# Performance work log

Measured on AMD Instinct MI355X. Metric: run time of the kernel, lower is better.

## Reference

```python
import jax, jax.numpy as jnp
import numpy as np

INPUT_DIM = 2048
EMBED_DIM = 128


def setup_inputs() -> dict:
    key = jax.random.key(0)
    kx, kw, kb, kv = jax.random.split(key, 4)
    x = jax.random.normal(kx, (16384, INPUT_DIM), dtype=jnp.float32)
    # nn.Linear(input_dim, 1): weight [1, D] (init std=0.01), bias [1]
    W = jax.random.normal(kw, (1, INPUT_DIM), dtype=jnp.float32) * 0.01
    b = jax.random.normal(kb, (1,), dtype=jnp.float32) * 0.01
    # nn.Embedding(input_dim, embedding_dim): V [D, K] (init std=0.01)
    V = jax.random.normal(kv, (INPUT_DIM, EMBED_DIM), dtype=jnp.float32) * 0.01
    return {"x": x, "W": W, "b": b, "V": V}


def reference(x, W, b, V):
    # linear part: x @ W^T + b -> [B, 1]
    linear_part = x @ W.T + b
    # FM 2nd-order interaction via the standard identity:
    # 0.5 * sum_k ( (sum_d x_d V_dk)^2 - sum_d x_d^2 V_dk^2 )
    # equals the original sum_square - square_sum over weighted embeddings.
    xv = x @ V                       # [B, K]
    x2v2 = (x * x) @ (V * V)         # [B, K]
    interaction = 0.5 * jnp.sum(xv * xv - x2v2, axis=1, keepdims=True)
    return linear_part + interaction
```

## Files before the change

### kernel.cpp

```cpp
#include <hip/hip_runtime.h>
#include <hip/hip_bf16.h>

#define INPUT_DIM 2048
#define EMBED_DIM 128
#define NROWS 16384

typedef __bf16 bf16x8 __attribute__((ext_vector_type(8)));
typedef float f32x4 __attribute__((ext_vector_type(4)));

__device__ inline float dot4(f32x4 a, f32x4 b) {
    return a.x * b.x + a.y * b.y + a.z * b.z + a.w * b.w;
}

__global__ __launch_bounds__(256) void fm_prep(const float* __restrict__ V,
                                               __bf16* __restrict__ Vt,
                                               float* __restrict__ s) {
    const int bid = blockIdx.x;
    const int tid = threadIdx.x;
    if (bid < 128) {
        const int g = bid * 256 + tid;
        const int n = g & 127;
        const int kc = g >> 7;
        bf16x8 o;
#pragma unroll
        for (int e = 0; e < 8; ++e)
            o[e] = (__bf16)V[(kc * 8 + e) * EMBED_DIM + n];
        *(bf16x8*)(Vt + (size_t)n * INPUT_DIM + kc * 8) = o;
    } else {
        const int k = (bid - 128) * 256 + tid;
        const f32x4* row = (const f32x4*)(V + (size_t)k * EMBED_DIM);
        float acc = 0.f;
#pragma unroll
        for (int j = 0; j < EMBED_DIM / 4; ++j) {
            f32x4 v = row[j];
            acc += dot4(v, v);
        }
        s[k] = acc;
    }
}

__global__ __launch_bounds__(256, 4) void fm_main(const float* __restrict__ x,
                                                  const float* __restrict__ W,
                                                  const float* __restrict__ bptr,
                                                  const __bf16* __restrict__ Vt,
                                                  const float* __restrict__ s,
                                                  float* __restrict__ out) {
    __shared__ __align__(16) float acc_lds[4][16][132];
    __shared__ float lin_lds[4][16];
    __shared__ float sq_lds[4][16];

    const int tid = threadIdx.x;
    const int w = tid >> 6;
    const int l = tid & 63;
    const int lr = l & 15;
    const int lg = l >> 4;

    const int row0 = blockIdx.x * 16;
    const int k0 = w * 512;

    const float* xp = x + (size_t)(row0 + lr) * INPUT_DIM + k0 + lg * 8;
    const float* wp = W + k0 + lg * 8;
    const float* sp = s + k0 + lg * 8;
    const __bf16* vtp = Vt + (size_t)lr * INPUT_DIM + k0 + lg * 8;

    f32x4 acc[8];
#pragma unroll
    for (int c = 0; c < 8; ++c) acc[c] = (f32x4){0.f, 0.f, 0.f, 0.f};
    float lin = 0.f, sq = 0.f;

    for (int step = 0; step < 16; ++step) {
        f32x4 a0 = *(const f32x4*)xp;
        f32x4 a1 = *(const f32x4*)(xp + 4);
        f32x4 w0 = *(const f32x4*)wp;
        f32x4 w1 = *(const f32x4*)(wp + 4);
        f32x4 s0 = *(const f32x4*)sp;
        f32x4 s1 = *(const f32x4*)(sp + 4);
        xp += 32; wp += 32; sp += 32;

        lin += dot4(a0, w0) + dot4(a1, w1);
        sq += dot4(a0 * a0, s0) + dot4(a1 * a1, s1);

        bf16x8 af;
        af[0] = (__bf16)a0.x; af[1] = (__bf16)a0.y;
        af[2] = (__bf16)a0.z; af[3] = (__bf16)a0.w;
        af[4] = (__bf16)a1.x; af[5] = (__bf16)a1.y;
        af[6] = (__bf16)a1.z; af[7] = (__bf16)a1.w;

#pragma unroll
        for (int c = 0; c < 8; ++c) {
            bf16x8 bf = *(const bf16x8*)(vtp + (size_t)c * 16 * INPUT_DIM);
            acc[c] = __builtin_amdgcn_mfma_f32_16x16x32_bf16(af, bf, acc[c], 0, 0, 0);
        }
        vtp += 32;
    }

#pragma unroll
    for (int c = 0; c < 8; ++c)
#pragma unroll
        for (int r = 0; r < 4; ++r)
            acc_lds[w][lg * 4 + r][c * 16 + lr] = acc[c][r];

    lin += __shfl_xor(lin, 16); lin += __shfl_xor(lin, 32);
    sq  += __shfl_xor(sq, 16);  sq  += __shfl_xor(sq, 32);
    if (l < 16) { lin_lds[w][l] = lin; sq_lds[w][l] = sq; }
    __syncthreads();

    {
        const int row = tid >> 4;
        const int nc = (tid & 15) * 8;
        f32x4 v0 = (f32x4){0.f, 0.f, 0.f, 0.f};
        f32x4 v1 = (f32x4){0.f, 0.f, 0.f, 0.f};
#pragma unroll
        for (int ww = 0; ww < 4; ++ww) {
            v0 += *(const f32x4*)&acc_lds[ww][row][nc];
            v1 += *(const f32x4*)&acc_lds[ww][row][nc + 4];
        }
        float ss = dot4(v0, v0) + dot4(v1, v1);
        ss += __shfl_xor(ss, 1);
        ss += __shfl_xor(ss, 2);
        ss += __shfl_xor(ss, 4);
        ss += __shfl_xor(ss, 8);
        if ((tid & 15) == 0) {
            float linf = lin_lds[0][row] + lin_lds[1][row] + lin_lds[2][row] + lin_lds[3][row];
            float sqf  = sq_lds[0][row] + sq_lds[1][row] + sq_lds[2][row] + sq_lds[3][row];
            out[row0 + row] = linf + bptr[0] + 0.5f * (ss - sqf);
        }
    }
}

extern "C" void kernel_launch(void* const* d_in, const int* in_sizes, int n_in,
                              void* d_out, int out_size, void* d_ws, size_t ws_size,
                              hipStream_t stream) {
    const float* x = (const float*)d_in[0];
    const float* W = (const float*)d_in[1];
    const float* b = (const float*)d_in[2];
    const float* V = (const float*)d_in[3];
    float* out = (float*)d_out;

    __bf16* Vt = (__bf16*)d_ws;
    float* s = (float*)((char*)d_ws + 128 * 2048 * sizeof(__bf16));

    fm_prep<<<136, 256, 0, stream>>>(V, Vt, s);
    fm_main<<<1024, 256, 0, stream>>>(x, W, b, Vt, s, out);
}
```

Measured before the change: 246.0 us.

## Prefetch x tiles in main loop and tile V transpose through LDS

```diff
diff --git a/kernel.cpp b/kernel.cpp
--- a/kernel.cpp
+++ b/kernel.cpp
@@ -15,31 +15,42 @@
 __global__ __launch_bounds__(256) void fm_prep(const float* __restrict__ V,
                                                __bf16* __restrict__ Vt,
                                                float* __restrict__ s) {
-    const int bid = blockIdx.x;
-    const int tid = threadIdx.x;
-    if (bid < 128) {
-        const int g = bid * 256 + tid;
-        const int n = g & 127;
-        const int kc = g >> 7;
-        bf16x8 o;
+    __shared__ float tile[64][132];
+    const int t = threadIdx.x;
+    const int k0 = blockIdx.x * 64;
+
 #pragma unroll
-        for (int e = 0; e < 8; ++e)
-            o[e] = (__bf16)V[(kc * 8 + e) * EMBED_DIM + n];
-        *(bf16x8*)(Vt + (size_t)n * INPUT_DIM + kc * 8) = o;
-    } else {
-        const int k = (bid - 128) * 256 + tid;
-        const f32x4* row = (const f32x4*)(V + (size_t)k * EMBED_DIM);
-        float acc = 0.f;
+    for (int i = 0; i < 8; ++i) {
+        int idx = i * 256 + t;
+        int kk = idx >> 5;
+        int nq = (idx & 31) * 4;
+        *(f32x4*)&tile[kk][nq] = *(const f32x4*)(V + (size_t)(k0 + kk) * EMBED_DIM + nq);
+    }
+    __syncthreads();
+
+    {
+        const int n = t >> 1;
+        const int ks = (t & 1) * 32;
+        __bf16 ov[32];
 #pragma unroll
-        for (int j = 0; j < EMBED_DIM / 4; ++j) {
-            f32x4 v = row[j];
-            acc += dot4(v, v);
+        for (int j = 0; j < 32; ++j) ov[j] = (__bf16)tile[ks + j][n];
+#pragma unroll
+        for (int q = 0; q < 4; ++q)
+            *(bf16x8*)(Vt + (size_t)n * INPUT_DIM + k0 + ks + q * 8) = *(bf16x8*)&ov[q * 8];
+    }
+
+    if (t < 64) {
+        float a = 0.f;
+#pragma unroll
+        for (int n4 = 0; n4 < 32; ++n4) {
+            f32x4 v = *(f32x4*)&tile[t][n4 * 4];
+            a += dot4(v, v);
         }
-        s[k] = acc;
+        s[k0 + t] = a;
     }
 }
 
-__global__ __launch_bounds__(256, 4) void fm_main(const float* __restrict__ x,
+__global__ __launch_bounds__(256, 3) void fm_main(const float* __restrict__ x,
                                                   const float* __restrict__ W,
                                                   const float* __restrict__ bptr,
                                                   const __bf16* __restrict__ Vt,
@@ -68,30 +79,49 @@
     for (int c = 0; c < 8; ++c) acc[c] = (f32x4){0.f, 0.f, 0.f, 0.f};
     float lin = 0.f, sq = 0.f;
 
+    f32x4 ca0 = *(const f32x4*)xp;
+    f32x4 ca1 = *(const f32x4*)(xp + 4);
+
+#pragma unroll 4
     for (int step = 0; step < 16; ++step) {
-        f32x4 a0 = *(const f32x4*)xp;
-        f32x4 a1 = *(const f32x4*)(xp + 4);
+        f32x4 na0 = ca0, na1 = ca1;
+        if (step < 15) {
+            na0 = *(const f32x4*)(xp + 32);
+            na1 = *(const f32x4*)(xp + 36);
+        }
+        bf16x8 vb0 = *(const bf16x8*)(vtp + 0 * 16 * INPUT_DIM);
+        bf16x8 vb1 = *(const bf16x8*)(vtp + 1 * 16 * INPUT_DIM);
+        bf16x8 vb2 = *(const bf16x8*)(vtp + 2 * 16 * INPUT_DIM);
+        bf16x8 vb3 = *(const bf16x8*)(vtp + 3 * 16 * INPUT_DIM);
+        bf16x8 vb4 = *(const bf16x8*)(vtp + 4 * 16 * INPUT_DIM);
+        bf16x8 vb5 = *(const bf16x8*)(vtp + 5 * 16 * INPUT_DIM);
+        bf16x8 vb6 = *(const bf16x8*)(vtp + 6 * 16 * INPUT_DIM);
+        bf16x8 vb7 = *(const bf16x8*)(vtp + 7 * 16 * INPUT_DIM);
         f32x4 w0 = *(const f32x4*)wp;
         f32x4 w1 = *(const f32x4*)(wp + 4);
         f32x4 s0 = *(const f32x4*)sp;
         f32x4 s1 = *(const f32x4*)(sp + 4);
-        xp += 32; wp += 32; sp += 32;
 
-        lin += dot4(a0, w0) + dot4(a1, w1);
-        sq += dot4(a0 * a0, s0) + dot4(a1 * a1, s1);
+        lin += dot4(ca0, w0) + dot4(ca1, w1);
+        sq += dot4(ca0 * ca0, s0) + dot4(ca1 * ca1, s1);
 
         bf16x8 af;
-        af[0] = (__bf16)a0.x; af[1] = (__bf16)a0.y;
-        af[2] = (__bf16)a0.z; af[3] = (__bf16)a0.w;
-        af[4] = (__bf16)a1.x; af[5] = (__bf16)a1.y;
-        af[6] = (__bf16)a1.z; af[7] = (__bf16)a1.w;
+        af[0] = (__bf16)ca0.x; af[1] = (__bf16)ca0.y;
+        af[2] = (__bf16)ca0.z; af[3] = (__bf16)ca0.w;
+        af[4] = (__bf16)ca1.x; af[5] = (__bf16)ca1.y;
+        af[6] = (__bf16)ca1.z; af[7] = (__bf16)ca1.w;
 
-#pragma unroll
-        for (int c = 0; c < 8; ++c) {
-            bf16x8 bf = *(const bf16x8*)(vtp + (size_t)c * 16 * INPUT_DIM);
-            acc[c] = __builtin_amdgcn_mfma_f32_16x16x32_bf16(af, bf, acc[c], 0, 0, 0);
-        }
-        vtp += 32;
+        acc[0] = __builtin_amdgcn_mfma_f32_16x16x32_bf16(af, vb0, acc[0], 0, 0, 0);
+        acc[1] = __builtin_amdgcn_mfma_f32_16x16x32_bf16(af, vb1, acc[1], 0, 0, 0);
+        acc[2] = __builtin_amdgcn_mfma_f32_16x16x32_bf16(af, vb2, acc[2], 0, 0, 0);
+        acc[3] = __builtin_amdgcn_mfma_f32_16x16x32_bf16(af, vb3, acc[3], 0, 0, 0);
+        acc[4] = __builtin_amdgcn_mfma_f32_16x16x32_bf16(af, vb4, acc[4], 0, 0, 0);
+        acc[5] = __builtin_amdgcn_mfma_f32_16x16x32_bf16(af, vb5, acc[5], 0, 0, 0);
+        acc[6] = __builtin_amdgcn_mfma_f32_16x16x32_bf16(af, vb6, acc[6], 0, 0, 0);
+        acc[7] = __builtin_amdgcn_mfma_f32_16x16x32_bf16(af, vb7, acc[7], 0, 0, 0);
+
+        ca0 = na0; ca1 = na1;
+        xp += 32; wp += 32; sp += 32; vtp += 32;
     }
 
 #pragma unroll
@@ -140,6 +170,6 @@
     __bf16* Vt = (__bf16*)d_ws;
     float* s = (float*)((char*)d_ws + 128 * 2048 * sizeof(__bf16));
 
-    fm_prep<<<136, 256, 0, stream>>>(V, Vt, s);
+    fm_prep<<<32, 256, 0, stream>>>(V, Vt, s);
     fm_main<<<1024, 256, 0, stream>>>(x, W, b, Vt, s, out);
 }
```

Result: no change. 250.5 us (+1.8%).
